# Kernel tuning notes

Hardware: AMD Instinct MI355X
Metric: run time of the kernel (lower is better)

Reference implementation:

```python
import jax, jax.numpy as jnp
from jax import lax
import numpy as np

ALPHA = 0.5
MAX_ITERS = 40
TOL = 1e-6
BITS = 8


def fake_quant_sym(w, bits=BITS):
    # symmetric per-tensor fake quantisation
    qmax = float(2 ** (bits - 1) - 1)
    scale = jnp.max(jnp.abs(w)) / qmax
    return jnp.round(w / scale) * scale


def fb_solve(Wq, Uq, bq, x, alpha=ALPHA, max_iters=MAX_ITERS, tol=TOL):
    # forward-backward splitting fixed-point solve: z = relu((1-a)z + a(Wz + Ux^T + b))
    n = Wq.shape[0]
    B = x.shape[0]
    Ux = Uq @ x.T + bq[:, None]  # (n, B), constant across iterations

    def cond(carry):
        z, res, it = carry
        return jnp.logical_and(it < max_iters, res >= tol)

    def body(carry):
        z, _, it = carry
        u = (1.0 - alpha) * z + alpha * (Wq @ z + Ux)
        z_next = jax.nn.relu(u)  # relu_prox
        res = jnp.linalg.norm(z_next - z) / (jnp.linalg.norm(z) + 1e-12)
        return z_next, res, it + 1

    z0 = jnp.zeros((n, B), dtype=x.dtype)
    z, _, _ = lax.while_loop(cond, body, (z0, jnp.array(jnp.inf, dtype=x.dtype), 0))
    u_star = (1.0 - alpha) * z + alpha * (Wq @ z + Ux)
    mask = (u_star > 0).astype(x.dtype)  # relu Jacobian mask D*
    return z, mask


def setup_inputs() -> dict:
    key = jax.random.key(0)
    k0, k1, k2, k3, k4 = jax.random.split(key, 5)
    n, d, B, C = 512, 784, 128, 10
    # scale W so ||W||_2 < 1 (monotone operator condition m > 0)
    W = 0.3 * jax.random.normal(k0, (n, n), dtype=jnp.float32) / jnp.sqrt(n)
    U = jax.random.normal(k1, (n, d), dtype=jnp.float32) / jnp.sqrt(d)
    b = 0.01 * jax.random.normal(k2, (n,), dtype=jnp.float32)
    x = jax.random.normal(k3, (B, d), dtype=jnp.float32)
    Wc = jax.random.normal(k4, (C, n), dtype=jnp.float32) / jnp.sqrt(n)
    bc = jnp.zeros((C,), dtype=jnp.float32)
    return {"W": W, "U": U, "b": b, "x": x, "Wc": Wc, "bc": bc}


def reference(W, U, b, x, Wc, bc):
    # post-training fake quantisation of W, U, b (done once at init in torch)
    Wq = fake_quant_sym(W)
    Uq = fake_quant_sym(U)
    bq = fake_quant_sym(b)
    z_star, _ = fb_solve(Wq, Uq, bq, x)  # (n, B)
    logits = z_star.T @ Wc.T + bc  # classifier on z*^T
    return logits
```

## Files before the change

kernel.cpp:

```cpp
#include <hip/hip_runtime.h>
#include <hip/hip_bf16.h>


#define N_DIM 512
#define D_DIM 784
#define B_DIM 128
#define C_DIM 10
#define QMAX 127.0f
#define N_ITERS 40
#define HILO_START 28
#define ZPITCH 528
#define MT 2
#define XPITCH 800
#define QUPITCH 808
#define MAGIC 8388608.0f

typedef int    i32x4  __attribute__((ext_vector_type(4)));
typedef float  f32x4  __attribute__((ext_vector_type(4)));
typedef float  f32x2  __attribute__((ext_vector_type(2)));
typedef __bf16 bf16x8 __attribute__((ext_vector_type(8)));

#define WSF_PW   0
#define WSF_PU   64
#define WSF_SB   128
#define WSF_CNTW 160
#define WSF_CNTU 224
#define WSF_BQ   288
#define WSF_XH   800
#define WSF_XL   (WSF_XH + 51200)
#define WSF_QP8  (WSF_XL + 51200)
#define WSF_UXT  (WSF_QP8 + 65536)

#define N_PW 64
#define N_PU 16

__device__ __forceinline__ float pscale64(const float* __restrict__ p) {
    float m = 0.0f;
#pragma unroll 16
    for (int i = 0; i < 64; ++i) m = fmaxf(m, p[i]);
    return m * (1.0f / QMAX);
}

__device__ __forceinline__ f32x2 pk_fma(f32x2 a, f32x2 b, f32x2 c) {
    f32x2 d;
    asm("v_pk_fma_f32 %0, %1, %2, %3" : "=v"(d) : "v"(a), "v"(b), "v"(c));
    return d;
}

__device__ __forceinline__ void pack_hl_f(float z0, float z1, float z2, float z3,
                                          unsigned int& h, unsigned int& l) {
    unsigned int f0 = __float_as_uint(z0 + MAGIC);
    unsigned int f1 = __float_as_uint(z1 + MAGIC);
    unsigned int f2 = __float_as_uint(z2 + MAGIC);
    unsigned int f3 = __float_as_uint(z3 + MAGIC);
    unsigned int m01 = __builtin_amdgcn_perm(f1, f0, 0x05040100u);
    unsigned int m23 = __builtin_amdgcn_perm(f3, f2, 0x05040100u);
    h = __builtin_amdgcn_perm(m23, m01, 0x07050301u);
    l = __builtin_amdgcn_perm(m23, m01, 0x06040200u) ^ 0x80808080u;
}

__global__ __launch_bounds__(256) void scales_kernel(const float* __restrict__ W,
                                                     const float* __restrict__ U,
                                                     const float* __restrict__ b,
                                                     const float* __restrict__ x,
                                                     float* __restrict__ ws) {
    __shared__ float ls[4];
    __shared__ float sbS;
    const int t = threadIdx.x, wave = t >> 6, lane = t & 63;
    const int bid = blockIdx.x;
    if (bid < 128) {
        const float4* src; int n4, rb;
        if (bid < 64) { src = (const float4*)W; n4 = N_DIM * N_DIM / 4; rb = bid; }
        else          { src = (const float4*)U; n4 = N_DIM * D_DIM / 4; rb = bid - 64; }
        float mv = 0.0f;
        for (int i = rb * 256 + t; i < n4; i += 64 * 256) {
            float4 v = src[i];
            mv = fmaxf(mv, fmaxf(fmaxf(fabsf(v.x), fabsf(v.y)), fmaxf(fabsf(v.z), fabsf(v.w))));
        }
#pragma unroll
        for (int s = 1; s < 64; s <<= 1) mv = fmaxf(mv, __shfl_xor(mv, s));
        if (lane == 0) ls[wave] = mv;
        __syncthreads();
        if (t == 0) ws[bid] = fmaxf(fmaxf(ls[0], ls[1]), fmaxf(ls[2], ls[3]));
    } else if (bid == 128) {
        if (t == 0) { ((int*)ws)[WSF_CNTW] = 0; ((int*)ws)[WSF_CNTU] = 0; }
        float4 v = {0.0f, 0.0f, 0.0f, 0.0f};
        if (t < N_DIM / 4) v = ((const float4*)b)[t];
        float mv = fmaxf(fmaxf(fabsf(v.x), fabsf(v.y)), fmaxf(fabsf(v.z), fabsf(v.w)));
#pragma unroll
        for (int s = 1; s < 64; s <<= 1) mv = fmaxf(mv, __shfl_xor(mv, s));
        if (lane == 0) ls[wave] = mv;
        __syncthreads();
        if (t == 0) {
            float m = fmaxf(fmaxf(ls[0], ls[1]), fmaxf(ls[2], ls[3]));
            float sb = m * (1.0f / QMAX);
            ws[WSF_SB] = sb;
            sbS = sb;
        }
        __syncthreads();
        if (t < N_DIM / 4) {
            const float sb = sbS;
            float4 o;
            o.x = rintf(v.x / sb) * sb;
            o.y = rintf(v.y / sb) * sb;
            o.z = rintf(v.z / sb) * sb;
            o.w = rintf(v.w / sb) * sb;
            ((float4*)(ws + WSF_BQ))[t] = o;
        }
    } else {
        __bf16* xh = (__bf16*)(ws + WSF_XH);
        __bf16* xl = (__bf16*)(ws + WSF_XL);
        const int xb = bid - 129;
        for (int i = xb * 256 + t; i < 128 * 196; i += 64 * 256) {
            int r = i / 196, kf = i - r * 196;
            float4 v = *(const float4*)&x[r * D_DIM + (kf << 2)];
            union { __bf16 e[4]; ushort4 u; } hh, ll;
            __bf16 h0 = (__bf16)v.x, h1 = (__bf16)v.y, h2 = (__bf16)v.z, h3 = (__bf16)v.w;
            hh.e[0] = h0; hh.e[1] = h1; hh.e[2] = h2; hh.e[3] = h3;
            ll.e[0] = (__bf16)(v.x - (float)h0);
            ll.e[1] = (__bf16)(v.y - (float)h1);
            ll.e[2] = (__bf16)(v.z - (float)h2);
            ll.e[3] = (__bf16)(v.w - (float)h3);
            *(ushort4*)&xh[r * XPITCH + (kf << 2)] = hh.u;
            *(ushort4*)&xl[r * XPITCH + (kf << 2)] = ll.u;
        }
        if (xb == 0) {
            int r = t >> 1, c = D_DIM + (t & 1) * 8;
            ushort4 z = {0, 0, 0, 0};
            *(ushort4*)&xh[r * XPITCH + c] = z; *(ushort4*)&xh[r * XPITCH + c + 4] = z;
            *(ushort4*)&xl[r * XPITCH + c] = z; *(ushort4*)&xl[r * XPITCH + c + 4] = z;
        }
    }
}

__global__ __launch_bounds__(1024, 1) void fused_kernel(const float* __restrict__ W,
                                                        const float* __restrict__ U,
                                                        float* __restrict__ ws,
                                                        const float* __restrict__ Wc,
                                                        const float* __restrict__ bc,
                                                        float* __restrict__ out) {
    __shared__ __align__(16) char LDS[54272];
    const int t = threadIdx.x;
    const int wave = t >> 6, lane = t & 63;
    const int bid = blockIdx.x;
    signed char* Qp8 = (signed char*)(ws + WSF_QP8);
    int* cntW = (int*)ws + WSF_CNTW;
    int* cntU = (int*)ws + WSF_CNTU;

    if (bid < 64) {
        const float s = pscale64(ws + WSF_PW);
        const float inv = 1.0f / s;
        int idx = bid * 1024 + t;
        float4 w = ((const float4*)W)[idx];
        int k = (idx << 2) & (N_DIM - 1);
        int r = (idx << 2) >> 9;
        char4 c;
        c.x = (signed char)(int)rintf(w.x * inv);
        c.y = (signed char)(int)rintf(w.y * inv);
        c.z = (signed char)(int)rintf(w.z * inv);
        c.w = (signed char)(int)rintf(w.w * inv);
        int kc = k >> 6, q = (k >> 4) & 3, jj = k & 15;
        *(char4*)&Qp8[((kc << 9) + r) * 64 + q * 16 + jj] = c;
        __syncthreads();
        if (t == 0) __hip_atomic_fetch_add(cntW, 1, __ATOMIC_RELEASE, __HIP_MEMORY_SCOPE_AGENT);
        return;
    }
    if (bid < 80) {
        __bf16 (*quS)[QUPITCH] = (__bf16 (*)[QUPITCH])LDS;
        const float sU = pscale64(ws + WSF_PU);
        const float invU = 1.0f / sU;
        const int i0 = (bid - 64) * 32;
        for (int i = t; i < 32 * 196; i += 1024) {
            int r = i / 196, kf = i - r * 196;
            float4 v = *(const float4*)&U[(i0 + r) * D_DIM + (kf << 2)];
            union { __bf16 e[4]; ushort4 u; } q;
            q.e[0] = (__bf16)rintf(v.x * invU);
            q.e[1] = (__bf16)rintf(v.y * invU);
            q.e[2] = (__bf16)rintf(v.z * invU);
            q.e[3] = (__bf16)rintf(v.w * invU);
            *(ushort4*)&quS[r][kf << 2] = q.u;
        }
        if (t < 512) { int r = t >> 4, k = D_DIM + (t & 15); quS[r][k] = (__bf16)0.0f; }
        __syncthreads();
        {
            const int m = lane & 15, quad = lane >> 4;
            const int rh = wave >> 3;
            const int cg = wave & 7;
            const __bf16* xh = (const __bf16*)(ws + WSF_XH);
            const __bf16* xl = (const __bf16*)(ws + WSF_XL);
            const float* bq = ws + WSF_BQ;
            float* UxT = ws + WSF_UXT;
            const int row0 = i0 + rh * 16 + (quad << 2);
            const f32x4 bqv = *(const f32x4*)&bq[row0];
            const __bf16* xhr = &xh[(cg * 16 + m) * XPITCH];
            const __bf16* xlr = &xl[(cg * 16 + m) * XPITCH];
            f32x4 acc = {};
#pragma unroll 5
            for (int kc = 0; kc < 25; ++kc) {
                bf16x8 au = *(const bf16x8*)&quS[rh * 16 + m][kc * 32 + (quad << 3)];
                bf16x8 bh = *(const bf16x8*)&xhr[kc * 32 + (quad << 3)];
                bf16x8 bl = *(const bf16x8*)&xlr[kc * 32 + (quad << 3)];
                acc = __builtin_amdgcn_mfma_f32_16x16x32_bf16(au, bh, acc, 0, 0, 0);
                acc = __builtin_amdgcn_mfma_f32_16x16x32_bf16(au, bl, acc, 0, 0, 0);
            }
            f32x4 o;
#pragma unroll
            for (int r = 0; r < 4; ++r) o[r] = sU * acc[r] + bqv[r];
            *(f32x4*)&UxT[(cg * 16 + m) * N_DIM + row0] = o;
        }
        __syncthreads();
        if (t == 0) __hip_atomic_fetch_add(cntU, 1, __ATOMIC_RELEASE, __HIP_MEMORY_SCOPE_AGENT);
        return;
    }

    signed char (*zh)[16][ZPITCH] = (signed char (*)[16][ZPITCH])(LDS);
    signed char (*zl)[16][ZPITCH] = (signed char (*)[16][ZPITCH])(LDS + 16896);
    float* WcS                    = (float*)(LDS + 33792);
    float (*red)[16][C_DIM]       = (float (*)[16][C_DIM])(LDS);
    const float* UxT = ws + WSF_UXT;
    const int m = lane & 15;
    const int quad = lane >> 4;
    const int c0 = (bid - 80) * 16;
    const float sW = pscale64(ws + WSF_PW);
    const float c1 = sW * (1.0f / 2048.0f);
    const float hc_hi = c1 * 128.0f;
    const float g_hi = sW * 128.0f;
    const float g_lo = sW * 0.5f;
    const int rowbase = wave * 32;

    for (int i = t; i < C_DIM * N_DIM; i += 1024) WcS[i] = Wc[i];

    if (t == 0) {
        while (__hip_atomic_load(cntW, __ATOMIC_RELAXED, __HIP_MEMORY_SCOPE_AGENT) < N_PW)
            __builtin_amdgcn_s_sleep(8);
    }
    __syncthreads();
    (void)__hip_atomic_load(cntW, __ATOMIC_ACQUIRE, __HIP_MEMORY_SCOPE_AGENT);

    i32x4 A[MT][8];
#pragma unroll
    for (int ti = 0; ti < MT; ++ti)
#pragma unroll
        for (int kc = 0; kc < 8; ++kc)
            A[ti][kc] = *(const i32x4*)&Qp8[((kc << 9) + rowbase + ti * 16 + m) * 64 + (quad << 4)];

    const i32x4 onesb = {0x01010101, 0x01010101, 0x01010101, 0x01010101};
    i32x4 rs[MT];
#pragma unroll
    for (int ti = 0; ti < MT; ++ti) {
        i32x4 a = {};
#pragma unroll
        for (int kc = 0; kc < 8; ++kc)
            a = __builtin_amdgcn_mfma_i32_16x16x64_i8(A[ti][kc], onesb, a, 0, 0, 0);
        rs[ti] = a;
    }

    if (t == 0) {
        while (__hip_atomic_load(cntU, __ATOMIC_RELAXED, __HIP_MEMORY_SCOPE_AGENT) < N_PU)
            __builtin_amdgcn_s_sleep(8);
    }
    __syncthreads();
    (void)__hip_atomic_load(cntU, __ATOMIC_ACQUIRE, __HIP_MEMORY_SCOPE_AGENT);

    f32x2 Zp[MT][2];
    f32x2 UX2p[MT][2];
#pragma unroll
    for (int ti = 0; ti < MT; ++ti) {
        const int row0 = rowbase + ti * 16 + (quad << 2);
        const f32x4 v4 = *(const f32x4*)&UxT[(c0 + m) * N_DIM + row0];
        float Zs[4];
#pragma unroll
        for (int r = 0; r < 4; ++r) {
            const float v = v4[r];
            const float uxh = 0.5f * (v + hc_hi * (float)rs[ti][r]);
            UX2p[ti][r >> 1][r & 1] = uxh * 2048.0f;
            const float z1 = fmaxf(0.5f * v, 0.0f);
            const float Z1 = z1 * 2048.0f;
            Zp[ti][r >> 1][r & 1] = Z1;
            Zs[r] = Z1;
        }
        unsigned int h, l;
        pack_hl_f(Zs[0], Zs[1], Zs[2], Zs[3], h, l);
        *(unsigned int*)&zh[0][m][row0] = h;
        *(unsigned int*)&zl[0][m][row0] = l;
    }

#pragma unroll
    for (int ti = 0; ti < MT; ++ti)
#pragma unroll
        for (int kc = 0; kc < 8; ++kc)
            asm volatile("" : "+v"(A[ti][kc]));
    __syncthreads();

    const f32x2 half2 = {0.5f, 0.5f};
    const f32x2 ghi2  = {g_hi, g_hi};
    const f32x2 glo2  = {g_lo, g_lo};

    int cur = 0;
    for (int it = 1; it < N_ITERS; ++it) {
        const bool lo = (it >= HILO_START);
        const bool wlo = (it >= HILO_START - 1);
        i32x4 acch[MT] = {};
        i32x4 accl[MT] = {};
        if (lo) {
#pragma unroll
            for (int kc = 0; kc < 8; ++kc) {
                const int ka = (kc << 6) + (quad << 4);
                i32x4 bh = *(const i32x4*)&zh[cur][m][ka];
                i32x4 bl = *(const i32x4*)&zl[cur][m][ka];
#pragma unroll
                for (int ti = 0; ti < MT; ++ti) {
                    acch[ti] = __builtin_amdgcn_mfma_i32_16x16x64_i8(A[ti][kc], bh, acch[ti], 0, 0, 0);
                    accl[ti] = __builtin_amdgcn_mfma_i32_16x16x64_i8(A[ti][kc], bl, accl[ti], 0, 0, 0);
                }
            }
        } else {
#pragma unroll
            for (int kc = 0; kc < 8; ++kc) {
                const int ka = (kc << 6) + (quad << 4);
                i32x4 bh = *(const i32x4*)&zh[cur][m][ka];
#pragma unroll
                for (int ti = 0; ti < MT; ++ti)
                    acch[ti] = __builtin_amdgcn_mfma_i32_16x16x64_i8(A[ti][kc], bh, acch[ti], 0, 0, 0);
            }
        }
        const int nxt = cur ^ 1;
#pragma unroll
        for (int ti = 0; ti < MT; ++ti) {
            const int row0 = rowbase + ti * 16 + (quad << 2);
            float Zs[4];
#pragma unroll
            for (int pr = 0; pr < 2; ++pr) {
                f32x2 base = pk_fma(half2, Zp[ti][pr], UX2p[ti][pr]);
                f32x2 inner = base;
                if (lo) {
                    f32x2 alf;
                    alf[0] = (float)accl[ti][2 * pr];
                    alf[1] = (float)accl[ti][2 * pr + 1];
                    inner = pk_fma(glo2, alf, base);
                }
                f32x2 ahf;
                ahf[0] = (float)acch[ti][2 * pr];
                ahf[1] = (float)acch[ti][2 * pr + 1];
                f32x2 u = pk_fma(ghi2, ahf, inner);
                float Zn0 = fmaxf(u[0], 0.0f);
                float Zn1 = fmaxf(u[1], 0.0f);
                Zp[ti][pr][0] = Zn0;
                Zp[ti][pr][1] = Zn1;
                Zs[2 * pr] = Zn0;
                Zs[2 * pr + 1] = Zn1;
            }
            unsigned int h, l;
            pack_hl_f(Zs[0], Zs[1], Zs[2], Zs[3], h, l);
            *(unsigned int*)&zh[nxt][m][row0] = h;
            if (wlo) *(unsigned int*)&zl[nxt][m][row0] = l;
        }
        __syncthreads();
        cur = nxt;
    }

    {
        float p[C_DIM];
#pragma unroll
        for (int cl = 0; cl < C_DIM; ++cl) p[cl] = 0.0f;
#pragma unroll
        for (int ti = 0; ti < MT; ++ti) {
            const int row0 = rowbase + ti * 16 + (quad << 2);
#pragma unroll
            for (int r = 0; r < 4; ++r) {
                float zv = Zp[ti][r >> 1][r & 1] * (1.0f / 2048.0f);
#pragma unroll
                for (int cl = 0; cl < C_DIM; ++cl)
                    p[cl] += zv * WcS[cl * N_DIM + row0 + r];
            }
        }
#pragma unroll
        for (int cl = 0; cl < C_DIM; ++cl) {
            p[cl] += __shfl_xor(p[cl], 16);
            p[cl] += __shfl_xor(p[cl], 32);
        }
        if (lane < 16) {
#pragma unroll
            for (int cl = 0; cl < C_DIM; ++cl) red[wave][lane][cl] = p[cl];
        }
        __syncthreads();
        for (int s = 8; s > 0; s >>= 1) {
            if (wave < s && lane < 16) {
#pragma unroll
                for (int cl = 0; cl < C_DIM; ++cl)
                    red[wave][lane][cl] += red[wave + s][lane][cl];
            }
            __syncthreads();
        }
        if (t < 16 * C_DIM) {
            int col = t & 15;
            int cl  = t >> 4;
            out[(c0 + col) * C_DIM + cl] = red[0][col][cl] + bc[cl];
        }
    }
}

extern "C" void kernel_launch(void* const* d_in, const int* in_sizes, int n_in,
                              void* d_out, int out_size, void* d_ws, size_t ws_size,
                              hipStream_t stream) {
    const float* W  = (const float*)d_in[0];
    const float* U  = (const float*)d_in[1];
    const float* b  = (const float*)d_in[2];
    const float* x  = (const float*)d_in[3];
    const float* Wc = (const float*)d_in[4];
    const float* bc = (const float*)d_in[5];
    float* out = (float*)d_out;
    float* ws = (float*)d_ws;

    scales_kernel<<<193, 256, 0, stream>>>(W, U, b, x, ws);
    fused_kernel<<<88, 1024, 0, stream>>>(W, U, ws, Wc, bc, out);
}
```

Measured before the change: 138.4 us.

## Split fixed-point loop into hi and hi/lo phases, batch LDS loads ahead of MFMAs

Splits the single iteration loop into two loops, one for the hi-only phase and one for the hi+lo phase, so the per-iteration branches go away. In each phase all B-operand LDS reads are issued into registers before the chain of int8 MFMAs, which lets load latency overlap with compute. The grid also grows from 88 to 96 blocks. Holding the preloaded operands raises register pressure, and the grid change may alter how work is split across blocks if the kernel does not derive that split from the block count.

```diff
diff --git a/kernel.cpp b/kernel.cpp
--- a/kernel.cpp
+++ b/kernel.cpp
@@ -297,33 +297,18 @@
     const f32x2 glo2  = {g_lo, g_lo};
 
     int cur = 0;
-    for (int it = 1; it < N_ITERS; ++it) {
-        const bool lo = (it >= HILO_START);
-        const bool wlo = (it >= HILO_START - 1);
+    for (int it = 1; it < HILO_START; ++it) {
+        const bool wlo = (it == HILO_START - 1);
+        i32x4 BH[8];
+#pragma unroll
+        for (int kc = 0; kc < 8; ++kc)
+            BH[kc] = *(const i32x4*)&zh[cur][m][(kc << 6) + (quad << 4)];
         i32x4 acch[MT] = {};
-        i32x4 accl[MT] = {};
-        if (lo) {
-#pragma unroll
-            for (int kc = 0; kc < 8; ++kc) {
-                const int ka = (kc << 6) + (quad << 4);
-                i32x4 bh = *(const i32x4*)&zh[cur][m][ka];
-                i32x4 bl = *(const i32x4*)&zl[cur][m][ka];
-#pragma unroll
-                for (int ti = 0; ti < MT; ++ti) {
-                    acch[ti] = __builtin_amdgcn_mfma_i32_16x16x64_i8(A[ti][kc], bh, acch[ti], 0, 0, 0);
-                    accl[ti] = __builtin_amdgcn_mfma_i32_16x16x64_i8(A[ti][kc], bl, accl[ti], 0, 0, 0);
-                }
-            }
-        } else {
-#pragma unroll
-            for (int kc = 0; kc < 8; ++kc) {
-                const int ka = (kc << 6) + (quad << 4);
-                i32x4 bh = *(const i32x4*)&zh[cur][m][ka];
-#pragma unroll
-                for (int ti = 0; ti < MT; ++ti)
-                    acch[ti] = __builtin_amdgcn_mfma_i32_16x16x64_i8(A[ti][kc], bh, acch[ti], 0, 0, 0);
-            }
-        }
+#pragma unroll
+        for (int kc = 0; kc < 8; ++kc)
+#pragma unroll
+            for (int ti = 0; ti < MT; ++ti)
+                acch[ti] = __builtin_amdgcn_mfma_i32_16x16x64_i8(A[ti][kc], BH[kc], acch[ti], 0, 0, 0);
         const int nxt = cur ^ 1;
 #pragma unroll
         for (int ti = 0; ti < MT; ++ti) {
@@ -332,13 +317,57 @@
 #pragma unroll
             for (int pr = 0; pr < 2; ++pr) {
                 f32x2 base = pk_fma(half2, Zp[ti][pr], UX2p[ti][pr]);
-                f32x2 inner = base;
-                if (lo) {
-                    f32x2 alf;
-                    alf[0] = (float)accl[ti][2 * pr];
-                    alf[1] = (float)accl[ti][2 * pr + 1];
-                    inner = pk_fma(glo2, alf, base);
+                f32x2 ahf;
+                ahf[0] = (float)acch[ti][2 * pr];
+                ahf[1] = (float)acch[ti][2 * pr + 1];
+                f32x2 u = pk_fma(ghi2, ahf, base);
+                float Zn0 = fmaxf(u[0], 0.0f);
+                float Zn1 = fmaxf(u[1], 0.0f);
+                Zp[ti][pr][0] = Zn0;
+                Zp[ti][pr][1] = Zn1;
+                Zs[2 * pr] = Zn0;
+                Zs[2 * pr + 1] = Zn1;
+            }
+            unsigned int h, l;
+            pack_hl_f(Zs[0], Zs[1], Zs[2], Zs[3], h, l);
+            *(unsigned int*)&zh[nxt][m][row0] = h;
+            if (wlo) *(unsigned int*)&zl[nxt][m][row0] = l;
+        }
+        __syncthreads();
+        cur = nxt;
+    }
+    for (int it = HILO_START; it < N_ITERS; ++it) {
+        i32x4 acch[MT] = {};
+        i32x4 accl[MT] = {};
+#pragma unroll
+        for (int g = 0; g < 2; ++g) {
+            i32x4 BH[4], BL[4];
+#pragma unroll
+            for (int j = 0; j < 4; ++j) {
+                const int ka = (((g << 2) + j) << 6) + (quad << 4);
+                BH[j] = *(const i32x4*)&zh[cur][m][ka];
+                BL[j] = *(const i32x4*)&zl[cur][m][ka];
+            }
+#pragma unroll
+            for (int j = 0; j < 4; ++j)
+#pragma unroll
+                for (int ti = 0; ti < MT; ++ti) {
+                    acch[ti] = __builtin_amdgcn_mfma_i32_16x16x64_i8(A[ti][(g << 2) + j], BH[j], acch[ti], 0, 0, 0);
+                    accl[ti] = __builtin_amdgcn_mfma_i32_16x16x64_i8(A[ti][(g << 2) + j], BL[j], accl[ti], 0, 0, 0);
                 }
+        }
+        const int nxt = cur ^ 1;
+#pragma unroll
+        for (int ti = 0; ti < MT; ++ti) {
+            const int row0 = rowbase + ti * 16 + (quad << 2);
+            float Zs[4];
+#pragma unroll
+            for (int pr = 0; pr < 2; ++pr) {
+                f32x2 base = pk_fma(half2, Zp[ti][pr], UX2p[ti][pr]);
+                f32x2 alf;
+                alf[0] = (float)accl[ti][2 * pr];
+                alf[1] = (float)accl[ti][2 * pr + 1];
+                f32x2 inner = pk_fma(glo2, alf, base);
                 f32x2 ahf;
                 ahf[0] = (float)acch[ti][2 * pr];
                 ahf[1] = (float)acch[ti][2 * pr + 1];
@@ -353,7 +382,7 @@
             unsigned int h, l;
             pack_hl_f(Zs[0], Zs[1], Zs[2], Zs[3], h, l);
             *(unsigned int*)&zh[nxt][m][row0] = h;
-            if (wlo) *(unsigned int*)&zl[nxt][m][row0] = l;
+            *(unsigned int*)&zl[nxt][m][row0] = l;
         }
         __syncthreads();
         cur = nxt;
@@ -413,5 +442,5 @@
     float* ws = (float*)d_ws;
 
     scales_kernel<<<193, 256, 0, stream>>>(W, U, b, x, ws);
-    fused_kernel<<<88, 1024, 0, stream>>>(W, U, ws, Wc, bc, out);
-}
+    fused_kernel<<<96, 1024, 0, stream>>>(W, U, ws, Wc, bc, out);
+}
```

Result: no change. 139.1 us (+0.5%).
